# Optimization experiments

Measured on AMD Instinct MI355X. Metric: run time of the kernel, lower is better.

## Reference

```python
import jax, jax.numpy as jnp
from jax import lax
import numpy as np

DN = ('NCHW', 'OIHW', 'NCHW')
EPS = 1e-8
LRELU_SLOPE = 0.2
SQRT2 = np.float32(np.sqrt(2.0))


def _blur2d(x):
    # 5x5 binomial FIR, depthwise, padding=2, stride=1 (Blur2d(kernel_size=5, padding=2))
    k1 = jnp.array([1.0, 4.0, 6.0, 4.0, 1.0], dtype=x.dtype)
    k2 = jnp.outer(k1, k1)
    k2 = k2 / k2.sum()
    C = x.shape[1]
    kern = jnp.broadcast_to(k2, (C, 1, 5, 5))
    return lax.conv_general_dilated(x, kern, window_strides=(1, 1),
                                    padding=[(2, 2), (2, 2)],
                                    feature_group_count=C,
                                    dimension_numbers=DN)


def _second_moment_norm(x, g):
    # normalize by per-channel spatial second moment, learnable gain g [C]
    ms = jnp.mean(jnp.square(x), axis=(2, 3), keepdims=True)  # [B,C,1,1]
    return x * lax.rsqrt(ms + EPS) * g[None, :, None, None]


def _modulated_conv(x, w, b, style_w, style_b, s, stride, padding):
    # StyleGAN2 modulated conv with demodulation, grouped-conv batch trick
    B, I, H, W = x.shape
    O, _, kh, kw = w.shape
    scale = np.float32(1.0 / np.sqrt(I * kh * kw))
    style = s @ style_w.T + style_b[None, :]                      # [B, I]
    wm = scale * w[None] * style[:, None, :, None, None]          # [B,O,I,kh,kw]
    d = lax.rsqrt(jnp.sum(jnp.square(wm), axis=(2, 3, 4)) + EPS)  # [B,O]
    wm = wm * d[:, :, None, None, None]
    xg = x.reshape(1, B * I, H, W)
    wg = wm.reshape(B * O, I, kh, kw)
    out = lax.conv_general_dilated(xg, wg, window_strides=(stride, stride),
                                   padding=[(padding, padding), (padding, padding)],
                                   feature_group_count=B,
                                   dimension_numbers=DN)
    out = out.reshape(B, O, out.shape[2], out.shape[3])
    return out + b[None, :, None, None]


def setup_inputs() -> dict:
    key = jax.random.key(0)
    ks = jax.random.split(key, 5)
    B, I, O, S, H, W, K = 8, 256, 256, 512, 128, 128, 3
    x = jax.random.normal(ks[0], (B, I, H, W), dtype=jnp.float32)
    s = jax.random.normal(ks[1], (B, S), dtype=jnp.float32)
    conv_w = jax.random.normal(ks[2], (O, I, K, K), dtype=jnp.float32)
    conv_b = jnp.zeros((O,), dtype=jnp.float32)
    style_w = jax.random.normal(ks[3], (I, S), dtype=jnp.float32) / np.float32(np.sqrt(S))
    style_b = jnp.ones((I,), dtype=jnp.float32)  # StyleGAN2 init: bias=1
    norm_g = jnp.ones((I,), dtype=jnp.float32)
    return {"x": x, "s": s, "conv_w": conv_w, "conv_b": conv_b,
            "style_w": style_w, "style_b": style_b, "norm_g": norm_g}


def reference(x, s, conv_w, conv_b, style_w, style_b, norm_g):
    x = _blur2d(x)                                   # blur (stride != 1 path)
    x = _second_moment_norm(x, norm_g)               # second-moment norm
    x = _modulated_conv(x, conv_w, conv_b, style_w, style_b, s, stride=2, padding=1)
    x = jnp.where(x >= 0, x, LRELU_SLOPE * x) * SQRT2  # scaled LeakyReLU
    return x
```

## Files before the change

### kernel.cpp

```cpp
#include <hip/hip_runtime.h>
#include <hip/hip_bf16.h>
#include <math.h>

#define B 8
#define IC 256
#define OC 256
#define SDIM 512
#define H 128
#define W 128
#define OH 64
#define OW 64
#define EPS 1e-8f
#define SQRT2 1.41421356237309504880f
#define SCALE 0.02083333395421505f

#define RS 16640
#define PLANE 1081600

typedef unsigned short u16;
typedef unsigned int u32;
typedef __attribute__((ext_vector_type(8))) short s16x8;
typedef __attribute__((ext_vector_type(4))) float f32x4;

__device__ __forceinline__ void gl_lds16(const void* g, void* l) {
    __builtin_amdgcn_global_load_lds((const __attribute__((address_space(1))) u32*)g,
                                     (__attribute__((address_space(3))) u32*)l, 16, 0, 0);
}

__global__ void wsq_kernel(const float* __restrict__ w, float* __restrict__ wsq,
                           float* __restrict__ zbuf) {
    int i = blockIdx.x * 256 + threadIdx.x;
    const float* p = w + (size_t)i * 9;
    float sum = 0.f;
    for (int k = 0; k < 9; ++k) sum = fmaf(p[k], p[k], sum);
    wsq[i] = sum;
    if (blockIdx.x == 0 && threadIdx.x < 64) zbuf[threadIdx.x] = 0.f;
}

__global__ __launch_bounds__(256) void style_demod_kernel(const float* __restrict__ s,
                                                          const float* __restrict__ sw,
                                                          const float* __restrict__ sb,
                                                          const float* __restrict__ wsq,
                                                          float* __restrict__ style,
                                                          float* __restrict__ demod,
                                                          float* __restrict__ ssq) {
    __shared__ float st[256];
    const int b = blockIdx.x;
    const int tid = threadIdx.x;
    const float4* sv = (const float4*)(s + (size_t)b * SDIM);
    const float4* wv = (const float4*)(sw + (size_t)tid * SDIM);
    float sum = 0.f;
    #pragma unroll 4
    for (int k = 0; k < 128; ++k) {
        float4 a4 = sv[k], b4 = wv[k];
        sum = fmaf(a4.x, b4.x, fmaf(a4.y, b4.y, fmaf(a4.z, b4.z, fmaf(a4.w, b4.w, sum))));
    }
    float styv = sum + sb[tid];
    style[(b << 8) + tid] = styv;
    st[tid] = styv;
    ssq[(b << 8) + tid] = 0.f;
    __syncthreads();
    const float4* wq = (const float4*)(wsq + (size_t)tid * 256);
    float acc = 0.f;
    #pragma unroll 4
    for (int k = 0; k < 64; ++k) {
        float4 q = wq[k];
        float s0 = st[4 * k], s1 = st[4 * k + 1], s2 = st[4 * k + 2], s3 = st[4 * k + 3];
        acc = fmaf(s0 * s0, q.x, fmaf(s1 * s1, q.y, fmaf(s2 * s2, q.z, fmaf(s3 * s3, q.w, acc))));
    }
    demod[(b << 8) + tid] = rsqrtf(SCALE * SCALE * acc + EPS);
}

__global__ __launch_bounds__(256, 5) void blurpack_kernel(const float* __restrict__ x,
                                                          __hip_bfloat16* __restrict__ xbp,
                                                          float* __restrict__ ssq,
                                                          const float* __restrict__ zbuf) {
    __shared__ __align__(16) char smem[32768];
    u16 (*pbuf)[2][2][544] = reinterpret_cast<u16(*)[2][2][544]>(smem);
    const float* rawf = (const float*)smem;
    const int strip = blockIdx.x;
    const int ic0 = blockIdx.y << 3;
    const int b = blockIdx.z;
    const int t = threadIdx.x;

    {
        int gidx = t ^ ((t >> 3) & 7);
        int sch = gidx >> 5, cg5 = gidx & 31;
        const float* xch = x + (((size_t)(b * 256 + ic0 + sch)) << 14) + (cg5 << 2);
        char* dst = smem + t * 16;
        #pragma unroll
        for (int k = 0; k < 8; ++k) {
            int gr = (strip << 2) - 2 + k;
            const void* src = (gr >= 0 && gr < H) ? (const void*)(xch + ((size_t)gr << 7))
                                                  : (const void*)zbuf;
            gl_lds16(src, dst + (k << 12));
        }
    }
    __syncthreads();

    const int hr = t >> 7;
    const int ch = (t >> 4) & 7;
    const int cg = t & 15;
    const int i0 = (ch << 5) + (cg << 1);
    const int p0 = i0 ^ ((i0 >> 3) & 7);
    const int p1 = p0 ^ 1;
    float ssacc = 0.f;
    uint2 res0[2], res1[2];

    #pragma unroll
    for (int pass = 0; pass < 2; ++pass) {
        const int br = (pass << 1) + hr;

        float v[8];
        #pragma unroll
        for (int j = 0; j < 8; ++j) v[j] = 0.f;
        #pragma unroll
        for (int rr = 0; rr < 5; ++rr) {
            const float wv = (rr == 2) ? 6.f : ((rr & 1) ? 4.f : 1.f);
            const int rb = (br + rr) << 10;
            float4 q0 = *(const float4*)(rawf + rb + (p0 << 2));
            float4 q1 = *(const float4*)(rawf + rb + (p1 << 2));
            v[0] = fmaf(wv, q0.x, v[0]); v[1] = fmaf(wv, q0.y, v[1]);
            v[2] = fmaf(wv, q0.z, v[2]); v[3] = fmaf(wv, q0.w, v[3]);
            v[4] = fmaf(wv, q1.x, v[4]); v[5] = fmaf(wv, q1.y, v[5]);
            v[6] = fmaf(wv, q1.z, v[6]); v[7] = fmaf(wv, q1.w, v[7]);
        }

        float vm2 = __shfl_up(v[6], 1, 64);
        float vm1 = __shfl_up(v[7], 1, 64);
        float vp1 = __shfl_down(v[0], 1, 64);
        float vp2 = __shfl_down(v[1], 1, 64);
        if (cg == 0)  { vm2 = 0.f; vm1 = 0.f; }
        if (cg == 15) { vp1 = 0.f; vp2 = 0.f; }
        float e[12];
        e[0] = vm2; e[1] = vm1;
        #pragma unroll
        for (int j = 0; j < 8; ++j) e[2 + j] = v[j];
        e[10] = vp1; e[11] = vp2;

        u16 hp[8];
        #pragma unroll
        for (int j = 0; j < 8; ++j) {
            float hv = fmaf(6.f, e[j + 2], fmaf(4.f, e[j + 1] + e[j + 3], e[j] + e[j + 4]))
                     * (1.0f / 256.0f);
            ssacc = fmaf(hv, hv, ssacc);
            __hip_bfloat16 hb = __float2bfloat16(hv);
            hp[j] = *(u16*)&hb;
        }
        u16 w0[4] = {hp[0], hp[2], hp[4], hp[6]};
        u16 w1[4] = {hp[1], hp[3], hp[5], hp[7]};
        res0[pass] = *(const uint2*)w0;
        res1[pass] = *(const uint2*)w1;
    }

    __syncthreads();

    #pragma unroll
    for (int pass = 0; pass < 2; ++pass) {
        *(uint2*)&pbuf[pass][hr][0][(ch << 6) + (cg << 2)] = res0[pass];
        *(uint2*)&pbuf[pass][hr][1][(ch << 6) + (cg << 2)] = res1[pass];
    }
    __syncthreads();

    {
        int fc = t & 127;
        int hr2 = t >> 7;
        int pw = fc & 1, pcol = fc >> 1;
        #pragma unroll
        for (int pass = 0; pass < 2; ++pass) {
            uint4 g;
            u16* gp = (u16*)&g;
            #pragma unroll
            for (int c2 = 0; c2 < 8; ++c2)
                gp[c2] = pbuf[pass][hr2][pw][(c2 << 6) + pcol];
            size_t off = (size_t)((b << 2) + (hr2 << 1) + pw) * PLANE
                       + (size_t)((strip << 1) + pass + 1) * RS
                       + (size_t)(pcol + 1) * 256 + ic0;
            *(uint4*)(xbp + off) = g;
        }
    }

    float sv2 = ssacc;
    sv2 += __shfl_down(sv2, 8, 16);
    sv2 += __shfl_down(sv2, 4, 16);
    sv2 += __shfl_down(sv2, 2, 16);
    sv2 += __shfl_down(sv2, 1, 16);
    if (cg == 0) atomicAdd(&ssq[(b << 8) + ic0 + ch], sv2);
}

__global__ void wf_kernel(const float* __restrict__ w,
                          const float* __restrict__ demod,
                          const float* __restrict__ ssq,
                          const float* __restrict__ style,
                          const float* __restrict__ g,
                          __hip_bfloat16* __restrict__ wf,
                          __hip_bfloat16* __restrict__ xbp) {
    int bo = blockIdx.x;
    int b = bo >> 8, o = bo & 255;
    int ic = threadIdx.x;
    float fac = rsqrtf(ssq[(b << 8) + ic] * (1.0f / 16384.0f) + EPS)
              * g[ic] * style[(b << 8) + ic] * SCALE;
    float m = demod[bo] * fac;
    const float* wp = w + ((size_t)o * 256 + ic) * 9;
    __hip_bfloat16* dst = wf + (size_t)bo * 2304 + ic;
    #pragma unroll
    for (int t = 0; t < 9; ++t)
        dst[t * 256] = __float2bfloat16(wp[t] * m);

    if (bo < 32) {
        int t = threadIdx.x;
        char* base = (char*)(xbp + (size_t)bo * PLANE);
        uint4 z = {0u, 0u, 0u, 0u};
        for (int k = 0; k < 9; ++k) {
            int c = t + (k << 8);
            if (c < 2080) *(uint4*)(base + (size_t)c * 16) = z;
        }
        for (int k = 0; k < 8; ++k) {
            int c = t + (k << 8);
            int r = 1 + (c >> 5);
            int off = (c & 31) << 3;
            *(uint4*)(base + ((size_t)r * RS + off) * 2) = z;
        }
    }
}

__global__ __launch_bounds__(256, 2) void conv_kernel(const __hip_bfloat16* __restrict__ xbp,
                                                      const __hip_bfloat16* __restrict__ wf,
                                                      const float* __restrict__ bias,
                                                      float* __restrict__ out) {
    __shared__ char lds[65536];
    const int t = threadIdx.x;
    const int o0 = blockIdx.x << 7;
    const int y  = blockIdx.y;
    const int b  = blockIdx.z;
    const size_t bb = (size_t)b << 8;

    u32 aoffs[4], boffs[4];
    #pragma unroll
    for (int j = 0; j < 4; ++j) {
        int s = t + (j << 8);
        int r = s >> 3, m = s & 7;
        int g = m ^ (r & 7);
        aoffs[j] = (u32)(r * 2304 + (g << 3)) * 2;
        boffs[j] = (u32)((((y << 1) + (r >> 6)) * RS) + ((r & 63) << 8) + (g << 3)) * 2;
    }
    const char* gAbase = (const char*)(wf + (bb + o0) * 2304);

    const int lane = t & 63, wave = t >> 6;
    const int lr = lane & 15, quad = lane >> 4;
    const int mb = (wave & 1) << 6;
    const int nb = (wave >> 1) << 6;

    f32x4 acc[4][4];
    #pragma unroll
    for (int i = 0; i < 4; ++i)
        #pragma unroll
        for (int j = 0; j < 4; ++j) acc[i][j] = (f32x4){0.f, 0.f, 0.f, 0.f};

    #define STAGE_TILE(cc, bufbase)                                                        \
    {                                                                                      \
        int tap = (cc) >> 2;                                                               \
        int icq = ((cc) & 3) << 6;                                                         \
        int th = (tap * 11) >> 5;                                                          \
        int tw = tap - th * 3;                                                             \
        int ph  = (th == 1) ? 0 : 1;                                                       \
        int dhp = (th == 0) ? 0 : 1;                                                       \
        int pw  = (tw == 1) ? 0 : 1;                                                       \
        int dwp = (tw == 0) ? 0 : 1;                                                       \
        const char* gA = gAbase + (size_t)(tap * 256 + icq) * 2;                           \
        const char* gB = (const char*)(xbp + (size_t)((b << 2) + (ph << 1) + pw) * PLANE   \
                                       + (size_t)dhp * RS + (dwp << 8) + icq);             \
        char* dA = (bufbase) + t * 16;                                                     \
        char* dB = (bufbase) + 16384 + t * 16;                                             \
        _Pragma("unroll")                                                                  \
        for (int j = 0; j < 4; ++j) gl_lds16(gA + aoffs[j], dA + (j << 12));               \
        _Pragma("unroll")                                                                  \
        for (int j = 0; j < 4; ++j) gl_lds16(gB + boffs[j], dB + (j << 12));               \
    }

    STAGE_TILE(0, lds);
    __syncthreads();

    int cur = 0;
    for (int c = 0; c < 36; ++c) {
        if (c < 35) STAGE_TILE(c + 1, lds + ((cur ^ 1) << 15));

        const char* ldsA = lds + (cur << 15);
        const char* ldsB = ldsA + 16384;
        #pragma unroll
        for (int s = 0; s < 2; ++s) {
            const int mq = ((s << 2) + quad) ^ (lr & 7);
            s16x8 a[4], bf[4];
            #pragma unroll
            for (int i = 0; i < 4; ++i)
                a[i] = *(const s16x8*)(ldsA + ((mb + (i << 4) + lr) << 7) + (mq << 4));
            #pragma unroll
            for (int j = 0; j < 4; ++j)
                bf[j] = *(const s16x8*)(ldsB + ((nb + (j << 4) + lr) << 7) + (mq << 4));
            #pragma unroll
            for (int i = 0; i < 4; ++i)
                #pragma unroll
                for (int j = 0; j < 4; ++j)
                    acc[i][j] = __builtin_amdgcn_mfma_f32_16x16x32_bf16(a[i], bf[j], acc[i][j], 0, 0, 0);
        }
        __syncthreads();
        cur ^= 1;
    }
    #undef STAGE_TILE

    float bi[4][4];
    #pragma unroll
    for (int i = 0; i < 4; ++i)
        #pragma unroll
        for (int rr = 0; rr < 4; ++rr)
            bi[i][rr] = bias[o0 + mb + (i << 4) + (quad << 2) + rr];
    const int n0 = y << 7;
    #pragma unroll
    for (int i = 0; i < 4; ++i) {
        #pragma unroll
        for (int j = 0; j < 4; ++j) {
            #pragma unroll
            for (int rr = 0; rr < 4; ++rr) {
                int oc = o0 + mb + (i << 4) + (quad << 2) + rr;
                int n = n0 + nb + (j << 4) + lr;
                int oh = n >> 6, ow2 = n & 63;
                float v = acc[i][j][rr] + bi[i][rr];
                v = (v >= 0.f ? v : 0.2f * v) * SQRT2;
                out[((bb + oc) << 12) + (oh << 6) + ow2] = v;
            }
        }
    }
}

extern "C" void kernel_launch(void* const* d_in, const int* in_sizes, int n_in,
                              void* d_out, int out_size, void* d_ws, size_t ws_size,
                              hipStream_t stream) {
    const float* x   = (const float*)d_in[0];
    const float* s   = (const float*)d_in[1];
    const float* cw  = (const float*)d_in[2];
    const float* cb  = (const float*)d_in[3];
    const float* sw  = (const float*)d_in[4];
    const float* sb  = (const float*)d_in[5];
    const float* ng  = (const float*)d_in[6];
    float* out = (float*)d_out;

    char* ws = (char*)d_ws;
    __hip_bfloat16* xbp = (__hip_bfloat16*)ws;
    __hip_bfloat16* wfb = (__hip_bfloat16*)(ws + 69222400);
    float* style  = (float*)(ws + 78659584);
    float* wsq    = style + 2048;
    float* demod  = wsq + 65536;
    float* ssq    = demod + 2048;
    float* zbuf   = ssq + 2048;

    wsq_kernel<<<256, 256, 0, stream>>>(cw, wsq, zbuf);
    style_demod_kernel<<<8, 256, 0, stream>>>(s, sw, sb, wsq, style, demod, ssq);
    blurpack_kernel<<<dim3(32, 32, 8), 256, 0, stream>>>(x, xbp, ssq, zbuf);
    wf_kernel<<<2048, 256, 0, stream>>>(cw, demod, ssq, style, ng, wfb, xbp);
    conv_kernel<<<dim3(2, 32, 8), 256, 0, stream>>>(xbp, wfb, cb, out);
}
```

Before: 308.6 us.

## Load weight fragments directly from global into registers, stage only activations in LDS

The A (modulated weight) operand is no longer staged through LDS. Each lane loads its MFMA fragments straight from global memory into registers, double-buffered across even and odd K-chunks, and only the B (activation) tile goes through LDS. This halves LDS use per block (64KB to 32KB) and removes the LDS write and read traffic for A, which could allow more blocks per CU. In exchange the loop needs many more vector registers, and the per-lane global reads of A are less coalesced and are duplicated across the two waves that share the same M rows.

```diff
diff --git a/kernel.cpp b/kernel.cpp
--- a/kernel.cpp
+++ b/kernel.cpp
@@ -228,36 +228,50 @@
                                                       const __hip_bfloat16* __restrict__ wf,
                                                       const float* __restrict__ bias,
                                                       float* __restrict__ out) {
-    __shared__ char lds[65536];
+    __shared__ char lds[32768];
     const int t = threadIdx.x;
     const int o0 = blockIdx.x << 7;
     const int y  = blockIdx.y;
     const int b  = blockIdx.z;
     const size_t bb = (size_t)b << 8;
 
-    u32 aoffs[4], boffs[4];
+    u32 boffs[4];
     #pragma unroll
     for (int j = 0; j < 4; ++j) {
         int s = t + (j << 8);
         int r = s >> 3, m = s & 7;
         int g = m ^ (r & 7);
-        aoffs[j] = (u32)(r * 2304 + (g << 3)) * 2;
         boffs[j] = (u32)((((y << 1) + (r >> 6)) * RS) + ((r & 63) << 8) + (g << 3)) * 2;
     }
-    const char* gAbase = (const char*)(wf + (bb + o0) * 2304);
 
     const int lane = t & 63, wave = t >> 6;
     const int lr = lane & 15, quad = lane >> 4;
     const int mb = (wave & 1) << 6;
     const int nb = (wave >> 1) << 6;
 
+    const char* gA[4];
+    #pragma unroll
+    for (int i = 0; i < 4; ++i)
+        gA[i] = (const char*)(wf + (bb + o0 + mb + (i << 4) + lr) * 2304) + (quad << 4);
+
     f32x4 acc[4][4];
     #pragma unroll
     for (int i = 0; i < 4; ++i)
         #pragma unroll
         for (int j = 0; j < 4; ++j) acc[i][j] = (f32x4){0.f, 0.f, 0.f, 0.f};
 
-    #define STAGE_TILE(cc, bufbase)                                                        \
+    #define KOFF(cc) ((((cc) >> 2) * 256 + (((cc) & 3) << 6)) * 2)
+
+    #define LOAD_A(cc, arr)                                                                \
+    {   const int ko_ = KOFF(cc);                                                          \
+        _Pragma("unroll")                                                                  \
+        for (int s_ = 0; s_ < 2; ++s_)                                                     \
+            _Pragma("unroll")                                                              \
+            for (int i_ = 0; i_ < 4; ++i_)                                                 \
+                arr[s_ * 4 + i_] = *(const s16x8*)(gA[i_] + ko_ + (s_ << 6));              \
+    }
+
+    #define STAGE_B(cc, bufbase)                                                           \
     {                                                                                      \
         int tap = (cc) >> 2;                                                               \
         int icq = ((cc) & 3) << 6;                                                         \
@@ -267,46 +281,56 @@
         int dhp = (th == 0) ? 0 : 1;                                                       \
         int pw  = (tw == 1) ? 0 : 1;                                                       \
         int dwp = (tw == 0) ? 0 : 1;                                                       \
-        const char* gA = gAbase + (size_t)(tap * 256 + icq) * 2;                           \
         const char* gB = (const char*)(xbp + (size_t)((b << 2) + (ph << 1) + pw) * PLANE   \
                                        + (size_t)dhp * RS + (dwp << 8) + icq);             \
-        char* dA = (bufbase) + t * 16;                                                     \
-        char* dB = (bufbase) + 16384 + t * 16;                                             \
-        _Pragma("unroll")                                                                  \
-        for (int j = 0; j < 4; ++j) gl_lds16(gA + aoffs[j], dA + (j << 12));               \
+        char* dB = (bufbase) + t * 16;                                                     \
         _Pragma("unroll")                                                                  \
         for (int j = 0; j < 4; ++j) gl_lds16(gB + boffs[j], dB + (j << 12));               \
     }
 
-    STAGE_TILE(0, lds);
+    #define COMPUTE(arr, bufbase)                                                          \
+    {                                                                                      \
+        _Pragma("unroll")                                                                  \
+        for (int s_ = 0; s_ < 2; ++s_) {                                                   \
+            const int mq_ = ((s_ << 2) + quad) ^ (lr & 7);                                 \
+            s16x8 bf_[4];                                                                  \
+            _Pragma("unroll")                                                              \
+            for (int j_ = 0; j_ < 4; ++j_)                                                 \
+                bf_[j_] = *(const s16x8*)((bufbase) + ((nb + (j_ << 4) + lr) << 7)         \
+                                          + (mq_ << 4));                                   \
+            _Pragma("unroll")                                                              \
+            for (int i_ = 0; i_ < 4; ++i_)                                                 \
+                _Pragma("unroll")                                                          \
+                for (int j_ = 0; j_ < 4; ++j_)                                             \
+                    acc[i_][j_] = __builtin_amdgcn_mfma_f32_16x16x32_bf16(                 \
+                        arr[s_ * 4 + i_], bf_[j_], acc[i_][j_], 0, 0, 0);                  \
+        }                                                                                  \
+    }
+
+    s16x8 aE[8], aO[8];
+    LOAD_A(0, aE);
+    STAGE_B(0, lds);
     __syncthreads();
 
     int cur = 0;
-    for (int c = 0; c < 36; ++c) {
-        if (c < 35) STAGE_TILE(c + 1, lds + ((cur ^ 1) << 15));
-
-        const char* ldsA = lds + (cur << 15);
-        const char* ldsB = ldsA + 16384;
-        #pragma unroll
-        for (int s = 0; s < 2; ++s) {
-            const int mq = ((s << 2) + quad) ^ (lr & 7);
-            s16x8 a[4], bf[4];
-            #pragma unroll
-            for (int i = 0; i < 4; ++i)
-                a[i] = *(const s16x8*)(ldsA + ((mb + (i << 4) + lr) << 7) + (mq << 4));
-            #pragma unroll
-            for (int j = 0; j < 4; ++j)
-                bf[j] = *(const s16x8*)(ldsB + ((nb + (j << 4) + lr) << 7) + (mq << 4));
-            #pragma unroll
-            for (int i = 0; i < 4; ++i)
-                #pragma unroll
-                for (int j = 0; j < 4; ++j)
-                    acc[i][j] = __builtin_amdgcn_mfma_f32_16x16x32_bf16(a[i], bf[j], acc[i][j], 0, 0, 0);
-        }
+    for (int cc = 0; cc < 36; cc += 2) {
+        STAGE_B(cc + 1, lds + ((cur ^ 1) << 14));
+        LOAD_A(cc + 1, aO);
+        COMPUTE(aE, lds + (cur << 14));
         __syncthreads();
         cur ^= 1;
-    }
-    #undef STAGE_TILE
+        if (cc + 2 < 36) {
+            STAGE_B(cc + 2, lds + ((cur ^ 1) << 14));
+            LOAD_A(cc + 2, aE);
+        }
+        COMPUTE(aO, lds + (cur << 14));
+        __syncthreads();
+        cur ^= 1;
+    }
+    #undef KOFF
+    #undef LOAD_A
+    #undef STAGE_B
+    #undef COMPUTE
 
     float bi[4][4];
     #pragma unroll
```

New measurement: 352.1 us. 1.14x slower.
